# Optimization experiments

Measured on AMD Instinct MI355X. Metric: run time of the kernel, lower is better.

## Reference

```python
import jax, jax.numpy as jnp
import numpy as np
from jax.scipy.linalg import solve_triangular

OMEGA0 = 30.0  # standard SIREN first-layer frequency


def setup_inputs() -> dict:
    key = jax.random.key(0)
    ks = jax.random.split(key, 12)
    B, NC, NT, XD, H, R = 64, 1024, 1024, 1, 512, 512
    x_context = jax.random.normal(ks[0], (B, NC, XD), jnp.float32)
    y_context = jax.random.normal(ks[1], (B, NC, 1), jnp.float32)
    x_target = jax.random.normal(ks[2], (B, NT, XD), jnp.float32)
    # SIREN MLP params (hidden_dims=[512,512,512], repr_dim=512)
    def lin(k, fi, fo, first=False):
        bound = 1.0 / fi if first else np.sqrt(6.0 / fi) / OMEGA0
        kW, kb = jax.random.split(k)
        W = jax.random.uniform(kW, (fi, fo), jnp.float32, -bound, bound)
        b = jax.random.uniform(kb, (fo,), jnp.float32, -bound, bound)
        return W, b
    W0, b0 = lin(ks[3], XD, H, first=True)
    W1, b1 = lin(ks[4], H, H)
    W2, b2 = lin(ks[5], H, H)
    Wr, br = lin(ks[6], H, R)
    log_noise_var = jnp.asarray(np.log(0.01), jnp.float32)
    return {"x_context": x_context, "y_context": y_context, "x_target": x_target,
            "W0": W0, "b0": b0, "W1": W1, "b1": b1, "W2": W2, "b2": b2,
            "Wr": Wr, "br": br, "log_noise_var": log_noise_var}


def _mlp(x, W0, b0, W1, b1, W2, b2, Wr, br):
    # SIREN: sine activations, omega_0 on first layer, linear head
    h = jnp.sin(OMEGA0 * (x @ W0 + b0))
    h = jnp.sin(h @ W1 + b1)
    h = jnp.sin(h @ W2 + b2)
    return h @ Wr + br


def reference(x_context, y_context, x_target, W0, b0, W1, b1, W2, b2, Wr, br, log_noise_var):
    mean = jnp.mean(y_context, axis=1, keepdims=True)          # [B,1,1]
    std = jnp.std(y_context, axis=1, keepdims=True, ddof=1)    # torch.std is unbiased
    yc = (y_context - mean) / std                              # [B,N,1]

    cr = _mlp(x_context, W0, b0, W1, b1, W2, b2, Wr, br)       # [B,N,R]
    tr = _mlp(x_target, W0, b0, W1, b1, W2, b2, Wr, br)        # [B,M,R]
    ones_c = jnp.ones(cr.shape[:-1] + (1,), cr.dtype)
    ones_t = jnp.ones(tr.shape[:-1] + (1,), tr.dtype)
    cr = jnp.concatenate([cr, ones_c], axis=-1)                # [B,N,R+1]
    tr = jnp.concatenate([tr, ones_t], axis=-1)                # [B,M,R+1]

    Rp1 = cr.shape[-1]
    cov = jnp.einsum('bnr,bns->brs', cr, cr)                   # [B,R+1,R+1]
    cov = cov + jnp.exp(log_noise_var) * jnp.eye(Rp1, dtype=cov.dtype)
    xty = jnp.einsum('bnr,bnd->brd', cr, yc)                   # [B,R+1,1]

    chol = jnp.linalg.cholesky(cov)                            # batched potrf
    z = solve_triangular(chol, xty, lower=True)
    w = solve_triangular(jnp.swapaxes(chol, -1, -2), z, lower=False)  # [B,R+1,1]

    y_pred = tr @ w                                            # [B,M,1]
    return y_pred * std + mean
```

## Files before the change

### kernel.cpp

```cpp
#include <hip/hip_runtime.h>
#include <hip/hip_fp16.h>
#include <math.h>

#define NB    64
#define NPTS  1024
#define HD    512
#define CPAD  576
#define COVE  ((size_t)NB*CPAD*CPAD)

typedef __attribute__((ext_vector_type(4))) float v4f;
typedef __attribute__((ext_vector_type(8))) short v8s;
typedef __attribute__((ext_vector_type(8))) _Float16 v8h;

__device__ __forceinline__ float sin_poly(float z){
  float t = z*z;
  float p = fmaf(t, -1.9841270e-4f, 8.3333333e-3f);
  p = fmaf(t, p, -0.16666667f);
  p = fmaf(t, p, 1.0f);
  return z*p;
}

__device__ __forceinline__ ushort2 split_f16(float a){
  _Float16 h = (_Float16)a;
  float hf = (float)h;
  _Float16 l = (_Float16)(a - hf);
  unsigned short uh, ul;
  __builtin_memcpy(&uh, &h, 2);
  __builtin_memcpy(&ul, &l, 2);
  ushort2 r; r.x = uh; r.y = ul;
  return r;
}

__device__ __forceinline__ unsigned short f16b(float a){
  _Float16 h = (_Float16)a;
  unsigned short uh; __builtin_memcpy(&uh, &h, 2);
  return uh;
}

__device__ __forceinline__ float f16r(float a){
  return (float)(_Float16)a;
}

__device__ __forceinline__ void g2l16(const unsigned short* g, unsigned short* l){
  __builtin_amdgcn_global_load_lds(
      (const __attribute__((address_space(1))) unsigned int*)(g),
      (__attribute__((address_space(3))) unsigned int*)(l), 16, 0, 0);
}

__global__ __launch_bounds__(256)
void prep_k(const float* __restrict__ W1, const float* __restrict__ W2,
            const float* __restrict__ Wr, unsigned short* __restrict__ wf)
{
  __shared__ unsigned short tile[64][65];
  const int mat = blockIdx.x >> 6;
  const int t = blockIdx.x & 63;
  const int k0 = (t >> 3)*64, n0 = (t & 7)*64;
  const float* W = (mat==0) ? W1 : ((mat==1) ? W2 : Wr);
  const int tid = threadIdx.x;
  for (int idx=tid; idx<4096; idx+=256){
    int r = idx >> 6, c = idx & 63;
    tile[r][c] = f16b(W[(size_t)(k0+r)*512 + n0 + c]);
  }
  __syncthreads();
  unsigned short* dst = wf + (size_t)mat*262144;
  for (int idx=tid; idx<4096; idx+=256){
    int r = idx >> 6, c = idx & 63;
    dst[(size_t)(n0+r)*512 + k0 + c] = tile[c][r];
  }
}

__device__ __forceinline__ void h0c(const float* __restrict__ w0,
                                    const float* __restrict__ b0, int K0, int sq,
                                    float xv0, float xv1, v8s& pa0, v8s& pa1)
{
  const float* wp = w0 + K0 + sq*8;
  const float* bp = b0 + K0 + sq*8;
  float4 wva = *(const float4*)wp, wvb = *(const float4*)(wp+4);
  float4 bva = *(const float4*)bp, bvb = *(const float4*)(bp+4);
  float w8[8] = {wva.x,wva.y,wva.z,wva.w,wvb.x,wvb.y,wvb.z,wvb.w};
  float b8[8] = {bva.x,bva.y,bva.z,bva.w,bvb.x,bvb.y,bvb.z,bvb.w};
  #pragma unroll
  for (int i=0;i<8;++i){
    pa0[i] = (short)f16b(__sinf(30.f*fmaf(xv0, w8[i], b8[i])));
    pa1[i] = (short)f16b(__sinf(30.f*fmaf(xv1, w8[i], b8[i])));
  }
}

template<int EPI, int TRANS, int AMODE>
__global__ __launch_bounds__(256)
void gemm_ld(const unsigned short* __restrict__ Ap,
             const float* __restrict__ xsrc, const float* __restrict__ w0,
             const float* __restrict__ b0,
             const unsigned short* __restrict__ Bw,
             const float* __restrict__ bias,
             unsigned short* __restrict__ Chi, unsigned short* __restrict__ Clo,
             const float* __restrict__ vvp, float* __restrict__ ydot, int rowBase)
{
  __shared__ unsigned short Ah[128*32], Bh[128*32];
  const int tid  = threadIdx.x;
  const int lane = tid & 63, wave = tid >> 6;
  const int wm = wave & 1, wn = wave >> 1;
  const int m0 = blockIdx.x*128, n0 = blockIdx.y*128;
  const int q = lane >> 4, ln16 = lane & 15;
  const int sr = tid >> 2, sq = tid & 3;

  const int strow = wave*32 + (lane>>2);
  const unsigned short* gA = Ap + (size_t)(m0 + strow)*512 + (lane&3)*8;
  const unsigned short* gB = Bw + (size_t)(n0 + strow)*512 + (lane&3)*8;
  unsigned short* lA0 = Ah + wave*1024;
  unsigned short* lB0 = Bh + wave*1024;

  float xv0 = 0.f, xv1 = 0.f;
  if (AMODE == 1){ xv0 = xsrc[m0 + sr]; xv1 = xsrc[m0 + sr + 64]; }

  v4f acc[4][4];
  #pragma unroll
  for (int a=0;a<4;++a)
    #pragma unroll
    for (int b=0;b<4;++b) acc[a][b] = (v4f)(0.0f);

  v8s pa0, pa1;
  if (AMODE == 1) h0c(w0, b0, 0, sq, xv0, xv1, pa0, pa1);

  for (int ks=0; ks<16; ++ks){
    const int k0 = ks*32;
    if (ks) __syncthreads();
    if (AMODE == 0){
      g2l16(gA + k0, lA0); g2l16(gA + k0 + 16*512, lA0 + 512);
    } else {
      *(v8s*)(Ah + sr*32 + sq*8) = pa0;
      *(v8s*)(Ah + (sr+64)*32 + sq*8) = pa1;
    }
    g2l16(gB + k0, lB0); g2l16(gB + k0 + 16*512, lB0 + 512);
    __syncthreads();
    if (AMODE == 1 && ks < 15)
      h0c(w0, b0, k0+32, sq, xv0, xv1, pa0, pa1);

    v8h bhf[4];
    #pragma unroll
    for (int nt=0; nt<4; ++nt){
      const int nrow = wn*64 + nt*16 + ln16;
      bhf[nt] = *(const v8h*)(Bh + nrow*32 + q*8);
    }
    #pragma unroll
    for (int mt=0; mt<4; ++mt){
      const int mrow = wm*64 + mt*16 + ln16;
      v8h ah = *(const v8h*)(Ah + mrow*32 + q*8);
      #pragma unroll
      for (int nt=0; nt<4; ++nt)
        acc[mt][nt] = __builtin_amdgcn_mfma_f32_16x16x32_f16(ah, bhf[nt], acc[mt][nt], 0,0,0);
    }
  }

  if (TRANS == 0){
    #pragma unroll
    for (int nt=0;nt<4;++nt){
      const int col = n0 + wn*64 + nt*16 + ln16;
      const float bl_ = bias[col];
      #pragma unroll
      for (int mt=0;mt<4;++mt){
        const int row0 = m0 + wm*64 + mt*16 + q*4;
        #pragma unroll
        for (int r=0;r<4;++r){
          float v = acc[mt][nt][r] + bl_;
          if (EPI == 1) v = sin_poly(v);
          Chi[(size_t)(row0+r)*512 + col] = f16b(v);
        }
      }
    }
  } else if (TRANS == 1){
    const int lb = m0 >> 10;
    #pragma unroll
    for (int nt=0;nt<4;++nt){
      const int col = n0 + wn*64 + nt*16 + ln16;
      const float bl_ = bias[col];
      #pragma unroll
      for (int mt=0;mt<4;++mt){
        const int row0 = m0 + wm*64 + mt*16 + q*4;
        const int nb = row0 & 1023;
        ushort4 h,l; ushort2 s;
        s=split_f16(acc[mt][nt][0]+bl_); h.x=s.x; l.x=s.y;
        s=split_f16(acc[mt][nt][1]+bl_); h.y=s.x; l.y=s.y;
        s=split_f16(acc[mt][nt][2]+bl_); h.z=s.x; l.z=s.y;
        s=split_f16(acc[mt][nt][3]+bl_); h.w=s.x; l.w=s.y;
        size_t o = ((size_t)lb*512 + col)*1024 + nb;
        *(ushort4*)(Chi + o) = h;
        *(ushort4*)(Clo + o) = l;
      }
    }
  } else {
    const int b = (rowBase + m0) >> 10;
    const float* vb = vvp + (size_t)b*512;
    float vcol[4];
    float bl_[4];
    #pragma unroll
    for (int nt=0;nt<4;++nt){
      const int col = n0 + wn*64 + nt*16 + ln16;
      vcol[nt] = vb[col];
      bl_[nt] = bias[col];
    }
    #pragma unroll
    for (int mt=0;mt<4;++mt){
      #pragma unroll
      for (int r=0;r<4;++r){
        float part = 0.f;
        #pragma unroll
        for (int nt=0;nt<4;++nt)
          part = fmaf(sin_poly(acc[mt][nt][r] + bl_[nt]), vcol[nt], part);
        #pragma unroll
        for (int off=1; off<16; off<<=1) part += __shfl_xor(part, off, 64);
        if (ln16 == 0){
          const int row = m0 + wm*64 + mt*16 + q*4 + r;
          atomicAdd(&ydot[rowBase + row], part);
        }
      }
    }
  }
}

__device__ __forceinline__ void ld_ext_row(const unsigned short* __restrict__ h,
                                           const unsigned short* __restrict__ l,
                                           const float* __restrict__ ycn,
                                           int f, int nofs, v8s& oh, v8s& ol)
{
  if (f < 512){
    oh = *(const v8s*)(h + (size_t)f*1024 + nofs);
    ol = *(const v8s*)(l + (size_t)f*1024 + nofs);
  } else if (f == 512){
    #pragma unroll
    for (int j=0;j<8;++j){ oh[j] = (short)0x3C00; ol[j] = 0; }
  } else if (f == 513){
    #pragma unroll
    for (int j=0;j<8;++j){
      ushort2 s = split_f16(ycn[nofs+j]);
      oh[j] = (short)s.x; ol[j] = (short)s.y;
    }
  } else {
    #pragma unroll
    for (int j=0;j<8;++j){ oh[j] = 0; ol[j] = 0; }
  }
}

__global__ __launch_bounds__(256)
void cov_ld(const unsigned short* __restrict__ CThi, const unsigned short* __restrict__ CTlo,
            const float* __restrict__ ycb,
            const float* __restrict__ lnv, float* __restrict__ cov, int bStart)
{
  int t = blockIdx.x;
  int ti = 0;
  while ((ti+1)*(ti+2)/2 <= t) ++ti;
  int tj = t - ti*(ti+1)/2;
  const int i0 = ti*128, j0 = tj*128;
  const int lb = blockIdx.y;
  const int b  = bStart + lb;
  const unsigned short* srch = CThi + (size_t)lb*512*1024;
  const unsigned short* srcl = CTlo + (size_t)lb*512*1024;
  const float* ycn = ycb + (size_t)b*NPTS;
  float* covb = cov + (size_t)b*CPAD*CPAD;
  const float noise = expf(lnv[0]);
  const bool diag = (i0 == j0);
  const bool aReg = (i0 == 512);

  __shared__ unsigned short Ah[128*32], Al[128*32], Bh2[128*32], Bl2[128*32];
  const int tid = threadIdx.x;
  const int lane = tid & 63, wave = tid >> 6;
  const int wm = wave & 1, wn = wave >> 1;
  const int q = lane >> 4, ln16 = lane & 15;
  const int sr = tid >> 2, sq = tid & 3;

  const int strow = wave*32 + (lane>>2);
  const size_t gaOff = (size_t)(i0 + strow)*1024 + (lane&3)*8;
  const size_t gbOff = (size_t)(j0 + strow)*1024 + (lane&3)*8;
  unsigned short* lA0 = Ah  + wave*1024;
  unsigned short* lL0 = Al  + wave*1024;
  unsigned short* lB0 = Bh2 + wave*1024;
  unsigned short* lM0 = Bl2 + wave*1024;

  v4f acc[4][4];
  #pragma unroll
  for (int a=0;a<4;++a)
    #pragma unroll
    for (int c=0;c<4;++c) acc[a][c] = (v4f)(0.0f);

  for (int ks=0; ks<32; ++ks){
    const int k0 = ks*32;
    if (ks) __syncthreads();
    if (!aReg){
      g2l16(srch + gaOff + k0, lA0); g2l16(srch + gaOff + k0 + (size_t)16*1024, lA0 + 512);
      g2l16(srcl + gaOff + k0, lL0); g2l16(srcl + gaOff + k0 + (size_t)16*1024, lL0 + 512);
    } else {
      v8s th, tl;
      ld_ext_row(srch, srcl, ycn, i0 + sr, k0 + sq*8, th, tl);
      *(v8s*)(Ah + sr*32 + sq*8) = th; *(v8s*)(Al + sr*32 + sq*8) = tl;
      ld_ext_row(srch, srcl, ycn, i0 + sr + 64, k0 + sq*8, th, tl);
      *(v8s*)(Ah + (sr+64)*32 + sq*8) = th; *(v8s*)(Al + (sr+64)*32 + sq*8) = tl;
    }
    if (!diag){
      g2l16(srch + gbOff + k0, lB0); g2l16(srch + gbOff + k0 + (size_t)16*1024, lB0 + 512);
      g2l16(srcl + gbOff + k0, lM0); g2l16(srcl + gbOff + k0 + (size_t)16*1024, lM0 + 512);
    }
    __syncthreads();

    const unsigned short* BhP = diag ? Ah : Bh2;
    const unsigned short* BlP = diag ? Al : Bl2;
    v8h bhf[4], blf[4];
    #pragma unroll
    for (int nt=0; nt<4; ++nt){
      const int nrow = wn*64 + nt*16 + ln16;
      bhf[nt] = *(const v8h*)(BhP + nrow*32 + q*8);
      blf[nt] = *(const v8h*)(BlP + nrow*32 + q*8);
    }
    #pragma unroll
    for (int mt=0; mt<4; ++mt){
      const int mrow = wm*64 + mt*16 + ln16;
      v8h ah = *(const v8h*)(Ah + mrow*32 + q*8);
      v8h al = *(const v8h*)(Al + mrow*32 + q*8);
      #pragma unroll
      for (int nt=0; nt<4; ++nt){
        acc[mt][nt] = __builtin_amdgcn_mfma_f32_16x16x32_f16(ah, bhf[nt], acc[mt][nt], 0,0,0);
        acc[mt][nt] = __builtin_amdgcn_mfma_f32_16x16x32_f16(ah, blf[nt], acc[mt][nt], 0,0,0);
        acc[mt][nt] = __builtin_amdgcn_mfma_f32_16x16x32_f16(al, bhf[nt], acc[mt][nt], 0,0,0);
      }
    }
  }
  #pragma unroll
  for (int nt=0;nt<4;++nt){
    const int gj = j0 + wn*64 + nt*16 + ln16;
    #pragma unroll
    for (int mt=0;mt<4;++mt){
      const int gi0 = i0 + wm*64 + mt*16 + q*4;
      #pragma unroll
      for (int r=0;r<4;++r){
        const int gi = gi0 + r;
        if (gj <= gi && gi < CPAD && gj < CPAD){
          float v = acc[mt][nt][r];
          if (gi == gj) v += (gi < 513) ? noise : 1.0f;
          covb[(size_t)gi*CPAD + gj] = v;
        }
      }
    }
  }
}

__global__ __launch_bounds__(256)
void chol_trsm_k(float* __restrict__ cov, float* __restrict__ dchol, int k)
{
  (void)dchol;
  float* Ab = cov + (size_t)blockIdx.x * CPAD * CPAD;
  const int o = k*64;
  const int row0 = o + 64 + blockIdx.y*128;
  const int nrows = min(128, CPAD - row0);
  __shared__ float Ds[64][65];
  __shared__ float As[128][65];
  __shared__ float invd[64];
  const int tid = threadIdx.x;

  for (int idx=tid; idx<1024; idx+=256){
    int r = idx >> 4, c = (idx & 15)*4;
    float4 v = *(const float4*)(Ab + (size_t)(o+r)*CPAD + o + c);
    Ds[r][c]   = (c   <= r) ? v.x : 0.f;
    Ds[r][c+1] = (c+1 <= r) ? v.y : 0.f;
    Ds[r][c+2] = (c+2 <= r) ? v.z : 0.f;
    Ds[r][c+3] = (c+3 <= r) ? v.w : 0.f;
  }
  for (int idx=tid; idx<nrows*16; idx+=256){
    int r = idx >> 4, c = (idx & 15)*4;
    float4 v = *(const float4*)(Ab + (size_t)(row0+r)*CPAD + o + c);
    As[r][c]=v.x; As[r][c+1]=v.y; As[r][c+2]=v.z; As[r][c+3]=v.w;
  }
  __syncthreads();

  for (int j=0; j<64; ++j){
    const float rp = 1.0f / Ds[j][j];
    const int i = j + 1 + (tid & 63);
    if (i < 64){
      const float t = Ds[i][j] * rp;
      for (int c = j+1+(tid>>6); c <= i; c += 4)
        Ds[i][c] = fmaf(-t, Ds[c][j], Ds[i][c]);
    }
    __syncthreads();
  }
  if (tid < 64) invd[tid] = 1.0f / sqrtf(Ds[tid][tid]);
  __syncthreads();
  for (int idx=tid; idx<4096; idx+=256){
    int r = idx >> 6, c = idx & 63;
    if (c <= r) Ds[r][c] *= invd[c];
  }
  __syncthreads();

  if (tid < nrows){
    float x[64];
    #pragma unroll
    for (int c=0; c<64; ++c){
      float s0 = As[tid][c], s1 = 0.f, s2 = 0.f, s3 = 0.f;
      #pragma unroll
      for (int j=0; j+4<=c; j+=4){
        s0 = fmaf(-x[j],   Ds[c][j],   s0);
        s1 = fmaf(-x[j+1], Ds[c][j+1], s1);
        s2 = fmaf(-x[j+2], Ds[c][j+2], s2);
        s3 = fmaf(-x[j+3], Ds[c][j+3], s3);
      }
      #pragma unroll
      for (int j = c & ~3; j < c; ++j)
        s0 = fmaf(-x[j], Ds[c][j], s0);
      x[c] = ((s0+s1)+(s2+s3)) * invd[c];
    }
    #pragma unroll
    for (int c=0; c<64; ++c) As[tid][c] = x[c];
  } else if (blockIdx.y == 0 && tid >= 128 && tid < 192){
    const int r = tid - 128;
    float y[64];
    #pragma unroll
    for (int c = 63; c >= 0; --c){
      float s0 = (c == r) ? 1.0f : 0.0f, s1 = 0.f, s2 = 0.f, s3 = 0.f;
      #pragma unroll
      for (int j = c+1; j+4 <= 64; j += 4){
        s0 = fmaf(-Ds[j][c],   y[j],   s0);
        s1 = fmaf(-Ds[j+1][c], y[j+1], s1);
        s2 = fmaf(-Ds[j+2][c], y[j+2], s2);
        s3 = fmaf(-Ds[j+3][c], y[j+3], s3);
      }
      #pragma unroll
      for (int j = c+1 + ((63-c) & ~3); j < 64; ++j)
        s0 = fmaf(-Ds[j][c], y[j], s0);
      y[c] = ((s0+s1)+(s2+s3)) * invd[c];
    }
    float* dst = Ab + (size_t)(o + r)*CPAD + 512;
    #pragma unroll
    for (int c = 0; c < 64; c += 4)
      *(float4*)(dst + c) = make_float4(y[c], y[c+1], y[c+2], y[c+3]);
  }
  __syncthreads();
  for (int idx=tid; idx<nrows*16; idx+=256){
    int r = idx >> 4, c = (idx & 15)*4;
    float4 v = make_float4(As[r][c], As[r][c+1], As[r][c+2], As[r][c+3]);
    *(float4*)(Ab + (size_t)(row0+r)*CPAD + o + c) = v;
  }
}

__global__ __launch_bounds__(256)
void chol_trail_k(float* __restrict__ cov, int k)
{
  float* Ab = cov + (size_t)blockIdx.y * CPAD * CPAD;
  int t = blockIdx.x;
  int bi = 0;
  while ((bi+1)*(bi+2)/2 <= t) ++bi;
  int bj = t - bi*(bi+1)/2;
  const int o = k*64;
  const int s0 = o + 64;
  const int I = s0 + bi*64, J = s0 + bj*64;

  __shared__ float Pi[64*64];
  __shared__ float Pj[64*64];
  const int tid = threadIdx.x;
  for (int idx = tid; idx < 1024; idx += 256){
    int r = idx >> 4, cq = idx & 15;
    float4 v = *(const float4*)(Ab + (size_t)(I+r)*CPAD + o + cq*4);
    Pi[(cq*4+0)*64 + r] = v.x; Pi[(cq*4+1)*64 + r] = v.y;
    Pi[(cq*4+2)*64 + r] = v.z; Pi[(cq*4+3)*64 + r] = v.w;
    float4 u = *(const float4*)(Ab + (size_t)(J+r)*CPAD + o + cq*4);
    Pj[(cq*4+0)*64 + r] = u.x; Pj[(cq*4+1)*64 + r] = u.y;
    Pj[(cq*4+2)*64 + r] = u.z; Pj[(cq*4+3)*64 + r] = u.w;
  }
  __syncthreads();
  const int tx = tid & 15, ty = tid >> 4;
  float acc[4][4];
  #pragma unroll
  for (int r=0;r<4;++r)
    #pragma unroll
    for (int c=0;c<4;++c) acc[r][c]=0.f;
  for (int kk=0; kk<64; ++kk){
    float4 a4 = *(const float4*)(Pi + kk*64 + tx*4);
    float4 b4 = *(const float4*)(Pj + kk*64 + ty*4);
    float av[4]={a4.x,a4.y,a4.z,a4.w}, bv[4]={b4.x,b4.y,b4.z,b4.w};
    #pragma unroll
    for (int r=0;r<4;++r)
      #pragma unroll
      for (int c=0;c<4;++c) acc[r][c] = fmaf(av[r], bv[c], acc[r][c]);
  }
  #pragma unroll
  for (int r=0;r<4;++r){
    int gi = I + tx*4 + r;
    #pragma unroll
    for (int c=0;c<4;++c){
      int gj = J + ty*4 + c;
      if (gj <= gi){
        size_t id = (size_t)gi*CPAD + gj;
        Ab[id] -= acc[r][c];
      }
    }
  }
}

__global__ __launch_bounds__(256)
void chol_last_k(float* __restrict__ cov, float* __restrict__ dchol)
{
  float* Ab = cov + (size_t)blockIdx.x * CPAD * CPAD;
  __shared__ float P[64][65];
  __shared__ float Ds[64][65];
  __shared__ float invl[64];
  const int tid = threadIdx.x;

  for (int idx=tid; idx<1024; idx+=256){
    int r = idx >> 4, c = (idx & 15)*4;
    float4 v = *(const float4*)(Ab + (size_t)(512+r)*CPAD + 448 + c);
    P[r][c]=v.x; P[r][c+1]=v.y; P[r][c+2]=v.z; P[r][c+3]=v.w;
    float4 u = *(const float4*)(Ab + (size_t)(512+r)*CPAD + 512 + c);
    Ds[r][c]   = (c   <= r) ? u.x : 0.f;
    Ds[r][c+1] = (c+1 <= r) ? u.y : 0.f;
    Ds[r][c+2] = (c+2 <= r) ? u.z : 0.f;
    Ds[r][c+3] = (c+3 <= r) ? u.w : 0.f;
  }
  __syncthreads();
  {
    const int tx = tid & 15, ty = tid >> 4;
    float acc[4][4];
    #pragma unroll
    for (int r=0;r<4;++r)
      #pragma unroll
      for (int c=0;c<4;++c) acc[r][c]=0.f;
    for (int kk=0; kk<64; ++kk){
      float av[4], bv[4];
      #pragma unroll
      for (int r=0;r<4;++r) av[r] = P[tx*4+r][kk];
      #pragma unroll
      for (int c=0;c<4;++c) bv[c] = P[ty*4+c][kk];
      #pragma unroll
      for (int r=0;r<4;++r)
        #pragma unroll
        for (int c=0;c<4;++c) acc[r][c] = fmaf(av[r], bv[c], acc[r][c]);
    }
    __syncthreads();
    #pragma unroll
    for (int r=0;r<4;++r){
      int gi = tx*4 + r;
      #pragma unroll
      for (int c=0;c<4;++c){
        int gj = ty*4 + c;
        if (gj <= gi) Ds[gi][gj] -= acc[r][c];
      }
    }
  }
  __syncthreads();

  for (int j=0; j<64; ++j){
    const float rp = 1.0f / Ds[j][j];
    const int i = j + 1 + (tid & 63);
    if (i < 64){
      const float t = Ds[i][j] * rp;
      for (int c = j+1+(tid>>6); c <= i; c += 4)
        Ds[i][c] = fmaf(-t, Ds[c][j], Ds[i][c]);
    }
    __syncthreads();
  }
  if (tid < 64) invl[tid] = 1.0f / sqrtf(Ds[tid][tid]);
  __syncthreads();
  for (int idx=tid; idx<4096; idx+=256){
    int r = idx >> 6, c = idx & 63;
    if (c <= r) Ds[r][c] *= invl[c];
  }
  __syncthreads();

  float* dst = dchol + ((size_t)blockIdx.x*9 + 8)*4096;
  for (int idx=tid; idx<4096; idx+=256)
    dst[idx] = Ds[idx>>6][idx&63];
  if (tid < 64){
    const int r = tid;
    float y[64];
    #pragma unroll
    for (int c = 63; c >= 0; --c){
      float s0 = (c == r) ? 1.0f : 0.0f, s1 = 0.f, s2 = 0.f, s3 = 0.f;
      #pragma unroll
      for (int j = c+1; j+4 <= 64; j += 4){
        s0 = fmaf(-Ds[j][c],   y[j],   s0);
        s1 = fmaf(-Ds[j+1][c], y[j+1], s1);
        s2 = fmaf(-Ds[j+2][c], y[j+2], s2);
        s3 = fmaf(-Ds[j+3][c], y[j+3], s3);
      }
      #pragma unroll
      for (int j = c+1 + ((63-c) & ~3); j < 64; ++j)
        s0 = fmaf(-Ds[j][c], y[j], s0);
      y[c] = ((s0+s1)+(s2+s3)) * invl[c];
    }
    float* dst2 = Ab + (size_t)(512 + r)*CPAD + 512;
    #pragma unroll
    for (int c = 0; c < 64; c += 4)
      *(float4*)(dst2 + c) = make_float4(y[c], y[c+1], y[c+2], y[c+3]);
  }
}

__global__ __launch_bounds__(1024)
void back_solve_k(const float* __restrict__ cov, const float* __restrict__ dchol,
                  float* __restrict__ wv)
{
  const int b = blockIdx.x;
  const float* L = cov + (size_t)b*CPAD*CPAD;
  const float* dc = dchol + (size_t)b*9*4096;
  __shared__ float inv2[64*64];
  __shared__ float rhs[CPAD];
  __shared__ float xv[64];
  __shared__ float red[4*512];
  const int tid = threadIdx.x;
  const int pr = tid >> 4, pc = (tid & 15)*4;
  const float* zrow = L + (size_t)513*CPAD;

  for (int i=tid; i<CPAD; i+=1024)
    rhs[i] = (i < 512) ? zrow[i] : ((i == 512) ? dc[8*4096 + 64] : 0.f);
  {
    float4 v = *(const float4*)(L + (size_t)(512 + pr)*CPAD + 512 + pc);
    *(float4*)(inv2 + pr*64 + pc) = v;
  }
  __syncthreads();

  for (int k=8; k>=1; --k){
    const int o = k*64;
    const int G = o >> 2;
    const int act = G << 2;
    float4 v16[16];
    int rg = 0, cg = 0;
    if (tid < act){
      rg = tid / G; cg = tid % G;
      const float* lp = L + (size_t)(o + rg*16)*CPAD + cg*4;
      #pragma unroll
      for (int rr=0; rr<16; ++rr)
        v16[rr] = *(const float4*)(lp + (size_t)rr*CPAD);
    }
    float4 pf = *(const float4*)(L + (size_t)((k-1)*64 + pr)*CPAD + 512 + pc);
    if (tid < 64){
      float acc = 0.f;
      #pragma unroll
      for (int j=0;j<64;++j) acc = fmaf(inv2[j*64 + tid], rhs[o+j], acc);
      xv[tid] = acc;
      rhs[o+tid] = acc;
    }
    __syncthreads();
    if (tid < act){
      float4 s = {0.f,0.f,0.f,0.f};
      #pragma unroll
      for (int rr=0; rr<16; ++rr){
        float xr = xv[rg*16 + rr];
        s.x = fmaf(v16[rr].x, xr, s.x);
        s.y = fmaf(v16[rr].y, xr, s.y);
        s.z = fmaf(v16[rr].z, xr, s.z);
        s.w = fmaf(v16[rr].w, xr, s.w);
      }
      *(float4*)(red + rg*512 + cg*4) = s;
    }
    __syncthreads();
    if (tid < o)
      rhs[tid] -= (red[tid] + red[512+tid]) + (red[1024+tid] + red[1536+tid]);
    *(float4*)(inv2 + pr*64 + pc) = pf;
    __syncthreads();
  }
  if (tid < 64){
    float acc = 0.f;
    #pragma unroll
    for (int j=0;j<64;++j) acc = fmaf(inv2[j*64 + tid], rhs[j], acc);
    rhs[tid] = acc;
  }
  __syncthreads();
  for (int i=tid; i<CPAD; i+=1024) wv[(size_t)b*CPAD + i] = rhs[i];
}

__global__ __launch_bounds__(512)
void fold_k(const float* __restrict__ Wr, const float* __restrict__ br,
            const float* __restrict__ wv, float* __restrict__ vv, float* __restrict__ cvec)
{
  int b = blockIdx.x, j = threadIdx.x;
  const float* wb = wv + (size_t)b*CPAD;
  __shared__ float ws_[512];
  __shared__ float red[512];
  ws_[j] = wb[j];
  __syncthreads();
  float acc = 0.f;
  const float* row = Wr + (size_t)j*512;
  for (int r=0; r<512; r+=4){
    float4 w4 = *(const float4*)(row + r);
    acc = fmaf(f16r(w4.x), ws_[r],   acc);
    acc = fmaf(f16r(w4.y), ws_[r+1], acc);
    acc = fmaf(f16r(w4.z), ws_[r+2], acc);
    acc = fmaf(f16r(w4.w), ws_[r+3], acc);
  }
  vv[(size_t)b*512 + j] = acc;
  red[j] = br[j]*ws_[j];
  __syncthreads();
  for (int s=256; s>0; s>>=1){ if (j<s) red[j]+=red[j+s]; __syncthreads(); }
  if (j == 0) cvec[b] = red[0] + wb[512];
}

__global__ __launch_bounds__(256)
void stats_k(const float* __restrict__ y, float* __restrict__ meanv,
             float* __restrict__ stdv, float* __restrict__ ycb)
{
  int b = blockIdx.x, tid = threadIdx.x;
  const float* yb = y + (size_t)b*NPTS;
  float4 v = *(const float4*)(yb + tid*4);
  float s  = v.x+v.y+v.z+v.w;
  float ss = v.x*v.x+v.y*v.y+v.z*v.z+v.w*v.w;
  #pragma unroll
  for (int off=32; off; off>>=1){ s += __shfl_down(s, off); ss += __shfl_down(ss, off); }
  __shared__ float rs[4], rss[4], bc[2];
  int wid = tid>>6, lane = tid&63;
  if (lane == 0){ rs[wid]=s; rss[wid]=ss; }
  __syncthreads();
  if (tid == 0){
    float S  = rs[0]+rs[1]+rs[2]+rs[3];
    float SS = rss[0]+rss[1]+rss[2]+rss[3];
    float mean = S * (1.0f/NPTS);
    float var  = (SS - S*S*(1.0f/NPTS)) * (1.0f/(NPTS-1));
    float sd = sqrtf(var);
    meanv[b]=mean; stdv[b]=sd; bc[0]=mean; bc[1]=1.0f/sd;
  }
  __syncthreads();
  float mean=bc[0], inv=bc[1];
  float4 o;
  o.x=(v.x-mean)*inv; o.y=(v.y-mean)*inv; o.z=(v.z-mean)*inv; o.w=(v.w-mean)*inv;
  *(float4*)(ycb + (size_t)b*NPTS + tid*4) = o;
}

__global__ __launch_bounds__(256)
void fin_k(const float* __restrict__ ydot, const float* __restrict__ cvec,
           const float* __restrict__ meanv, const float* __restrict__ stdv,
           float* __restrict__ out)
{
  int i = blockIdx.x*256 + threadIdx.x;
  int b = i >> 10;
  out[i] = fmaf(ydot[i] + cvec[b], stdv[b], meanv[b]);
}

extern "C" void kernel_launch(void* const* d_in, const int* in_sizes, int n_in,
                              void* d_out, int out_size, void* d_ws, size_t ws_size,
                              hipStream_t stream)
{
  (void)in_sizes; (void)n_in; (void)out_size;
  const float* x_ctx = (const float*)d_in[0];
  const float* y_ctx = (const float*)d_in[1];
  const float* x_tgt = (const float*)d_in[2];
  const float* W0 = (const float*)d_in[3];
  const float* b0 = (const float*)d_in[4];
  const float* W1 = (const float*)d_in[5];
  const float* b1 = (const float*)d_in[6];
  const float* W2 = (const float*)d_in[7];
  const float* b2 = (const float*)d_in[8];
  const float* Wr = (const float*)d_in[9];
  const float* br = (const float*)d_in[10];
  const float* lnv = (const float*)d_in[11];
  float* out = (float*)d_out;
  float* ws = (float*)d_ws;

  int CH = 65536;
  for (;;){
    size_t fl = COVE + 65536 + 192 + (size_t)64*512 + (size_t)64*CPAD + 65536
              + (size_t)64*9*4096 + 64;
    size_t sh = (size_t)3*262144 + (size_t)2*CH*512 + (size_t)2*(CH/1024)*512*1024;
    size_t need = fl*4 + sh*2;
    if (ws_size >= need || CH <= 1024) break;
    CH >>= 1;
  }
  const int nch = 65536 / CH;
  const int bpc = CH / NPTS;

  float* cov   = ws;
  float* ycb   = cov + COVE;
  float* meanv = ycb + 65536;
  float* stdv  = meanv + 64;
  float* cvec  = stdv + 64;
  float* vvb   = cvec + 64;
  float* wvb   = vvb + (size_t)64*512;
  float* ydot  = wvb + (size_t)64*CPAD;
  float* dchol = ydot + 65536;
  unsigned short* wf   = (unsigned short*)(dchol + (size_t)64*9*4096);
  unsigned short* P0   = wf + (size_t)3*262144;
  unsigned short* P1   = P0 + (size_t)CH*512;
  unsigned short* CThi = P1 + (size_t)CH*512;
  unsigned short* CTlo = CThi + (size_t)bpc*512*1024;

  prep_k<<<192, 256, 0, stream>>>(W1, W2, Wr, wf);
  stats_k<<<NB, 256, 0, stream>>>(y_ctx, meanv, stdv, ycb);

  for (int c=0; c<nch; ++c){
    const float* xc = x_ctx + (size_t)c*CH;
    dim3 g(CH/128, 4);
    gemm_ld<1,0,1><<<g, 256, 0, stream>>>(0, xc, W0, b0, wf, b1, P1, 0, 0, 0, 0);
    gemm_ld<1,0,0><<<g, 256, 0, stream>>>(P1, 0, 0, 0, wf+262144, b2, P0, 0, 0, 0, 0);
    gemm_ld<0,1,0><<<g, 256, 0, stream>>>(P0, 0, 0, 0, wf+524288, br, CThi, CTlo, 0, 0, 0);
    cov_ld<<<dim3(15, bpc), 256, 0, stream>>>(CThi, CTlo, ycb, lnv, cov, c*bpc);
  }

  for (int k=0; k<8; ++k){
    const int cnt = CPAD - k*64 - 64;
    chol_trsm_k<<<dim3(NB, (cnt + 127)/128), 256, 0, stream>>>(cov, dchol, k);
    if (k < 7){
      const int tcnt = cnt >> 6;
      chol_trail_k<<<dim3(tcnt*(tcnt+1)/2, NB), 256, 0, stream>>>(cov, k);
    }
  }
  chol_last_k<<<NB, 256, 0, stream>>>(cov, dchol);
  back_solve_k<<<NB, 1024, 0, stream>>>(cov, dchol, wvb);
  fold_k<<<NB, 512, 0, stream>>>(Wr, br, wvb, vvb, cvec);

  hipMemsetAsync(ydot, 0, 65536*sizeof(float), stream);
  for (int c=0; c<nch; ++c){
    const float* xt = x_tgt + (size_t)c*CH;
    dim3 g(CH/128, 4);
    gemm_ld<1,0,1><<<g, 256, 0, stream>>>(0, xt, W0, b0, wf, b1, P1, 0, 0, 0, 0);
    gemm_ld<1,2,0><<<g, 256, 0, stream>>>(P1, 0, 0, 0, wf+262144, b2, 0, 0, vvb, ydot, c*CH);
  }
  fin_k<<<256, 256, 0, stream>>>(ydot, cvec, meanv, stdv, out);
}
```

Baseline: 1.312 ms.

## Double-buffer LDS tiles with XOR swizzle in MLP and covariance GEMMs

Both the MLP GEMM and the covariance SYRK kernels now use two LDS buffers, so the next K-slice is loaded (global-to-LDS or computed sine/extended rows) while MFMAs run on the current one. This cuts the per-iteration sync count from two to one. LDS columns are also XOR-swizzled by row to reduce bank conflicts on the 16-byte fragment reads. The cost is double the LDS footprint, which may lower occupancy, especially in the covariance kernel, which now needs 64KB.

```diff
diff --git a/kernel.cpp b/kernel.cpp
--- a/kernel.cpp
+++ b/kernel.cpp
@@ -96,19 +96,20 @@
              unsigned short* __restrict__ Chi, unsigned short* __restrict__ Clo,
              const float* __restrict__ vvp, float* __restrict__ ydot, int rowBase)
 {
-  __shared__ unsigned short Ah[128*32], Bh[128*32];
+  __shared__ unsigned short Ah[2][4096], Bh[2][4096];
   const int tid  = threadIdx.x;
   const int lane = tid & 63, wave = tid >> 6;
   const int wm = wave & 1, wn = wave >> 1;
   const int m0 = blockIdx.x*128, n0 = blockIdx.y*128;
   const int q = lane >> 4, ln16 = lane & 15;
   const int sr = tid >> 2, sq = tid & 3;
+  const int qx  = (q ^ ((ln16>>1)&3))*8;
+  const int swc = ((lane&3) ^ ((lane>>3)&3))*8;
+  const int wsl = (sq ^ ((sr>>1)&3))*8;
 
   const int strow = wave*32 + (lane>>2);
-  const unsigned short* gA = Ap + (size_t)(m0 + strow)*512 + (lane&3)*8;
-  const unsigned short* gB = Bw + (size_t)(n0 + strow)*512 + (lane&3)*8;
-  unsigned short* lA0 = Ah + wave*1024;
-  unsigned short* lB0 = Bh + wave*1024;
+  const unsigned short* gA = Ap + (size_t)(m0 + strow)*512 + swc;
+  const unsigned short* gB = Bw + (size_t)(n0 + strow)*512 + swc;
 
   float xv0 = 0.f, xv1 = 0.f;
   if (AMODE == 1){ xv0 = xsrc[m0 + sr]; xv1 = xsrc[m0 + sr + 64]; }
@@ -120,36 +121,47 @@
     for (int b=0;b<4;++b) acc[a][b] = (v4f)(0.0f);
 
   v8s pa0, pa1;
-  if (AMODE == 1) h0c(w0, b0, 0, sq, xv0, xv1, pa0, pa1);
-
+  if (AMODE == 0){
+    g2l16(gA, Ah[0]+wave*1024); g2l16(gA+16*512, Ah[0]+wave*1024+512);
+  } else {
+    h0c(w0, b0, 0, sq, xv0, xv1, pa0, pa1);
+    *(v8s*)(Ah[0] + sr*32 + wsl) = pa0;
+    *(v8s*)(Ah[0] + (sr+64)*32 + wsl) = pa1;
+  }
+  g2l16(gB, Bh[0]+wave*1024); g2l16(gB+16*512, Bh[0]+wave*1024+512);
+  __syncthreads();
+
+  int cur = 0;
   for (int ks=0; ks<16; ++ks){
-    const int k0 = ks*32;
-    if (ks) __syncthreads();
-    if (AMODE == 0){
-      g2l16(gA + k0, lA0); g2l16(gA + k0 + 16*512, lA0 + 512);
-    } else {
-      *(v8s*)(Ah + sr*32 + sq*8) = pa0;
-      *(v8s*)(Ah + (sr+64)*32 + sq*8) = pa1;
-    }
-    g2l16(gB + k0, lB0); g2l16(gB + k0 + 16*512, lB0 + 512);
-    __syncthreads();
-    if (AMODE == 1 && ks < 15)
-      h0c(w0, b0, k0+32, sq, xv0, xv1, pa0, pa1);
-
+    const int nxt = cur^1;
+    if (ks < 15){
+      const int k1 = (ks+1)*32;
+      if (AMODE == 0){
+        g2l16(gA+k1, Ah[nxt]+wave*1024); g2l16(gA+k1+16*512, Ah[nxt]+wave*1024+512);
+      }
+      g2l16(gB+k1, Bh[nxt]+wave*1024); g2l16(gB+k1+16*512, Bh[nxt]+wave*1024+512);
+    }
     v8h bhf[4];
     #pragma unroll
     for (int nt=0; nt<4; ++nt){
       const int nrow = wn*64 + nt*16 + ln16;
-      bhf[nt] = *(const v8h*)(Bh + nrow*32 + q*8);
+      bhf[nt] = *(const v8h*)(Bh[cur] + nrow*32 + qx);
     }
     #pragma unroll
     for (int mt=0; mt<4; ++mt){
       const int mrow = wm*64 + mt*16 + ln16;
-      v8h ah = *(const v8h*)(Ah + mrow*32 + q*8);
+      v8h ah = *(const v8h*)(Ah[cur] + mrow*32 + qx);
       #pragma unroll
       for (int nt=0; nt<4; ++nt)
         acc[mt][nt] = __builtin_amdgcn_mfma_f32_16x16x32_f16(ah, bhf[nt], acc[mt][nt], 0,0,0);
     }
+    if (AMODE == 1 && ks < 15){
+      h0c(w0, b0, (ks+1)*32, sq, xv0, xv1, pa0, pa1);
+      *(v8s*)(Ah[nxt] + sr*32 + wsl) = pa0;
+      *(v8s*)(Ah[nxt] + (sr+64)*32 + wsl) = pa1;
+    }
+    __syncthreads();
+    cur = nxt;
   }
 
   if (TRANS == 0){
@@ -261,20 +273,20 @@
   const bool diag = (i0 == j0);
   const bool aReg = (i0 == 512);
 
-  __shared__ unsigned short Ah[128*32], Al[128*32], Bh2[128*32], Bl2[128*32];
+  __shared__ unsigned short Ah[2][4096], Al[2][4096], Bh2[2][4096], Bl2[2][4096];
   const int tid = threadIdx.x;
   const int lane = tid & 63, wave = tid >> 6;
   const int wm = wave & 1, wn = wave >> 1;
   const int q = lane >> 4, ln16 = lane & 15;
   const int sr = tid >> 2, sq = tid & 3;
+  const int qx  = (q ^ ((ln16>>1)&3))*8;
+  const int swc = ((lane&3) ^ ((lane>>3)&3))*8;
+  const int wsl = (sq ^ ((sr>>1)&3))*8;
 
   const int strow = wave*32 + (lane>>2);
-  const size_t gaOff = (size_t)(i0 + strow)*1024 + (lane&3)*8;
-  const size_t gbOff = (size_t)(j0 + strow)*1024 + (lane&3)*8;
-  unsigned short* lA0 = Ah  + wave*1024;
-  unsigned short* lL0 = Al  + wave*1024;
-  unsigned short* lB0 = Bh2 + wave*1024;
-  unsigned short* lM0 = Bl2 + wave*1024;
+  const size_t gaOff = (size_t)(i0 + strow)*1024 + swc;
+  const size_t gbOff = (size_t)(j0 + strow)*1024 + swc;
+  const int wb = wave*1024;
 
   v4f acc[4][4];
   #pragma unroll
@@ -282,39 +294,54 @@
     #pragma unroll
     for (int c=0;c<4;++c) acc[a][c] = (v4f)(0.0f);
 
+  if (!aReg){
+    g2l16(srch + gaOff, Ah[0]+wb); g2l16(srch + gaOff + (size_t)16*1024, Ah[0]+wb+512);
+    g2l16(srcl + gaOff, Al[0]+wb); g2l16(srcl + gaOff + (size_t)16*1024, Al[0]+wb+512);
+  } else {
+    v8s th, tl;
+    ld_ext_row(srch, srcl, ycn, i0 + sr, sq*8, th, tl);
+    *(v8s*)(Ah[0] + sr*32 + wsl) = th; *(v8s*)(Al[0] + sr*32 + wsl) = tl;
+    ld_ext_row(srch, srcl, ycn, i0 + sr + 64, sq*8, th, tl);
+    *(v8s*)(Ah[0] + (sr+64)*32 + wsl) = th; *(v8s*)(Al[0] + (sr+64)*32 + wsl) = tl;
+  }
+  if (!diag){
+    g2l16(srch + gbOff, Bh2[0]+wb); g2l16(srch + gbOff + (size_t)16*1024, Bh2[0]+wb+512);
+    g2l16(srcl + gbOff, Bl2[0]+wb); g2l16(srcl + gbOff + (size_t)16*1024, Bl2[0]+wb+512);
+  }
+  __syncthreads();
+
+  int cur = 0;
   for (int ks=0; ks<32; ++ks){
-    const int k0 = ks*32;
-    if (ks) __syncthreads();
-    if (!aReg){
-      g2l16(srch + gaOff + k0, lA0); g2l16(srch + gaOff + k0 + (size_t)16*1024, lA0 + 512);
-      g2l16(srcl + gaOff + k0, lL0); g2l16(srcl + gaOff + k0 + (size_t)16*1024, lL0 + 512);
-    } else {
-      v8s th, tl;
-      ld_ext_row(srch, srcl, ycn, i0 + sr, k0 + sq*8, th, tl);
-      *(v8s*)(Ah + sr*32 + sq*8) = th; *(v8s*)(Al + sr*32 + sq*8) = tl;
-      ld_ext_row(srch, srcl, ycn, i0 + sr + 64, k0 + sq*8, th, tl);
-      *(v8s*)(Ah + (sr+64)*32 + sq*8) = th; *(v8s*)(Al + (sr+64)*32 + sq*8) = tl;
-    }
-    if (!diag){
-      g2l16(srch + gbOff + k0, lB0); g2l16(srch + gbOff + k0 + (size_t)16*1024, lB0 + 512);
-      g2l16(srcl + gbOff + k0, lM0); g2l16(srcl + gbOff + k0 + (size_t)16*1024, lM0 + 512);
-    }
-    __syncthreads();
-
-    const unsigned short* BhP = diag ? Ah : Bh2;
-    const unsigned short* BlP = diag ? Al : Bl2;
+    const int nxt = cur^1;
+    if (ks < 31){
+      const int k1 = (ks+1)*32;
+      if (!aReg){
+        g2l16(srch + gaOff + k1, Ah[nxt]+wb);
+        g2l16(srch + gaOff + k1 + (size_t)16*1024, Ah[nxt]+wb+512);
+        g2l16(srcl + gaOff + k1, Al[nxt]+wb);
+        g2l16(srcl + gaOff + k1 + (size_t)16*1024, Al[nxt]+wb+512);
+      }
+      if (!diag){
+        g2l16(srch + gbOff + k1, Bh2[nxt]+wb);
+        g2l16(srch + gbOff + k1 + (size_t)16*1024, Bh2[nxt]+wb+512);
+        g2l16(srcl + gbOff + k1, Bl2[nxt]+wb);
+        g2l16(srcl + gbOff + k1 + (size_t)16*1024, Bl2[nxt]+wb+512);
+      }
+    }
+    const unsigned short* BhP = diag ? Ah[cur] : Bh2[cur];
+    const unsigned short* BlP = diag ? Al[cur] : Bl2[cur];
     v8h bhf[4], blf[4];
     #pragma unroll
     for (int nt=0; nt<4; ++nt){
       const int nrow = wn*64 + nt*16 + ln16;
-      bhf[nt] = *(const v8h*)(BhP + nrow*32 + q*8);
-      blf[nt] = *(const v8h*)(BlP + nrow*32 + q*8);
+      bhf[nt] = *(const v8h*)(BhP + nrow*32 + qx);
+      blf[nt] = *(const v8h*)(BlP + nrow*32 + qx);
     }
     #pragma unroll
     for (int mt=0; mt<4; ++mt){
       const int mrow = wm*64 + mt*16 + ln16;
-      v8h ah = *(const v8h*)(Ah + mrow*32 + q*8);
-      v8h al = *(const v8h*)(Al + mrow*32 + q*8);
+      v8h ah = *(const v8h*)(Ah[cur] + mrow*32 + qx);
+      v8h al = *(const v8h*)(Al[cur] + mrow*32 + qx);
       #pragma unroll
       for (int nt=0; nt<4; ++nt){
         acc[mt][nt] = __builtin_amdgcn_mfma_f32_16x16x32_f16(ah, bhf[nt], acc[mt][nt], 0,0,0);
@@ -322,6 +349,16 @@
         acc[mt][nt] = __builtin_amdgcn_mfma_f32_16x16x32_f16(al, bhf[nt], acc[mt][nt], 0,0,0);
       }
     }
+    if (aReg && ks < 31){
+      const int n1 = (ks+1)*32 + sq*8;
+      v8s th, tl;
+      ld_ext_row(srch, srcl, ycn, i0 + sr, n1, th, tl);
+      *(v8s*)(Ah[nxt] + sr*32 + wsl) = th; *(v8s*)(Al[nxt] + sr*32 + wsl) = tl;
+      ld_ext_row(srch, srcl, ycn, i0 + sr + 64, n1, th, tl);
+      *(v8s*)(Ah[nxt] + (sr+64)*32 + wsl) = th; *(v8s*)(Al[nxt] + (sr+64)*32 + wsl) = tl;
+    }
+    __syncthreads();
+    cur = nxt;
   }
   #pragma unroll
   for (int nt=0;nt<4;++nt){
```

Result: no change. 1.298 ms (-1.0%).
